# Optimization experiments

Hardware: AMD Instinct MI355X
Metric: run time of the kernel (lower is better)

## Reference

```python
import jax, jax.numpy as jnp
import numpy as np

N_NODES = 50000
N_EDGES = 1500000
FEAT = 128
CUTOFF = 5.0


def setup_inputs() -> dict:
    key = jax.random.key(0)
    k_x, k_ei, k_el, k_w = jax.random.split(key, 4)
    x = jax.random.normal(k_x, (N_NODES, FEAT), dtype=jnp.float32)
    edge_index = jax.random.randint(k_ei, (2, N_EDGES), 0, N_NODES, dtype=jnp.int64)
    edge_len = jax.random.uniform(k_el, (N_EDGES,), dtype=jnp.float32) * CUTOFF
    # learned params: equivariant mix (dense linear for scalar irreps, no bias),
    # log of distance scale (init sharpness=6.0), and 1->1 filter linear.
    W_mix = jax.random.normal(k_w, (FEAT, FEAT), dtype=jnp.float32) / np.sqrt(FEAT)
    log_scale = jnp.asarray(np.log(6.0), dtype=jnp.float32)
    filter_w = jnp.asarray(0.7, dtype=jnp.float32)
    filter_b = jnp.asarray(0.1, dtype=jnp.float32)
    return {"x": x, "edge_index": edge_index, "edge_len": edge_len,
            "W_mix": W_mix, "log_scale": log_scale,
            "filter_w": filter_w, "filter_b": filter_b}


def reference(x, edge_index, edge_len, W_mix, log_scale, filter_w, filter_b):
    sender = edge_index[0]
    receiver = edge_index[1]
    n_nodes = x.shape[0]

    scale = jnp.exp(log_scale).astype(edge_len.dtype)
    decay = jnp.exp(-jnp.maximum(edge_len / (scale + 1e-6), 0.0) ** 2)  # [E]
    gate = jax.nn.sigmoid(edge_len * filter_w + filter_b)               # [E]
    weights = jnp.nan_to_num(decay * gate, nan=0.0, posinf=0.0, neginf=0.0)

    # gather-scale-scatter: messages [E, F] -> per-node sum
    messages = weights[:, None].astype(x.dtype) * x[sender]
    agg = jax.ops.segment_sum(messages, receiver, num_segments=n_nodes)
    degree = jax.ops.segment_sum(jnp.ones_like(edge_len), receiver,
                                 num_segments=n_nodes)
    agg = agg / jnp.maximum(degree, 1.0)[:, None].astype(x.dtype)

    return x + agg @ W_mix
```

## Files before the change

kernel.cpp:

```cpp
#include <hip/hip_runtime.h>
#include <math.h>

#define FEAT 128
#define BSHIFT 5
#define BNODES 32
#define CAP 2048
#define EPB 8192
#define NBUCK_MAX 2048

__device__ __forceinline__ float edge_weight(float d, float scale, float fw, float fb) {
    float t = fmaxf(d / scale, 0.0f);
    float decay = expf(-t * t);
    float g = 1.0f / (1.0f + expf(-(d * fw + fb)));
    float w = decay * g;
    if (!isfinite(w)) w = 0.0f;
    return w;
}

__device__ __forceinline__ unsigned int bf16_rne(float f) {
    unsigned int b = __float_as_uint(f);
    return (b + 0x7FFFu + ((b >> 16) & 1u)) >> 16;
}

__global__ __launch_bounds__(256) void convert_kernel(const float4* __restrict__ x4,
                                                      uint2* __restrict__ xbf,
                                                      int n4) {
    int i = blockIdx.x * 256 + threadIdx.x;
    if (i >= n4) return;
    float4 v = x4[i];
    uint2 o;
    o.x = (bf16_rne(v.y) << 16) | bf16_rne(v.x);
    o.y = (bf16_rne(v.w) << 16) | bf16_rne(v.z);
    xbf[i] = o;
}

__global__ __launch_bounds__(256) void count_kernel(const int* __restrict__ recv,
                                                    int* __restrict__ boff,
                                                    int E, int nbuck) {
    __shared__ int cnt[NBUCK_MAX];
    int tid = threadIdx.x;
    for (int i = tid; i < nbuck; i += 256) cnt[i] = 0;
    __syncthreads();
    int base = blockIdx.x * EPB;
    int end = min(base + EPB, E);
    for (int e = base + tid; e < end; e += 256)
        atomicAdd(&cnt[recv[e] >> BSHIFT], 1);
    __syncthreads();
    for (int i = tid; i < nbuck; i += 256) {
        int c = cnt[i];
        if (c) atomicAdd(&boff[i + 1], c);
    }
}

__global__ __launch_bounds__(1024) void scan_kernel(int* __restrict__ off,
                                                    int* __restrict__ bcur, int M) {
    __shared__ int part[1024];
    int t = threadIdx.x;
    int chunk = (M + 1023) >> 10;
    int lo = t * chunk, hi = min(lo + chunk, M);
    int s = 0;
    for (int i = lo; i < hi; ++i) s += off[1 + i];
    part[t] = s;
    __syncthreads();
    for (int d = 1; d < 1024; d <<= 1) {
        int v = (t >= d) ? part[t - d] : 0;
        __syncthreads();
        part[t] += v;
        __syncthreads();
    }
    int run = part[t] - s;
    for (int i = lo; i < hi; ++i) {
        bcur[i] = run;
        run += off[1 + i];
        off[1 + i] = run;
    }
    if (t == 0) off[0] = 0;
}

__global__ __launch_bounds__(256) void bucket_scatter_kernel(
    const int* __restrict__ sender, const int* __restrict__ recv,
    const float* __restrict__ edge_len,
    const float* __restrict__ log_scale, const float* __restrict__ filter_w,
    const float* __restrict__ filter_b,
    int* __restrict__ bcur, unsigned long long* __restrict__ buf,
    int E, int nbuck) {
    __shared__ int cur[NBUCK_MAX];
    int tid = threadIdx.x;
    for (int i = tid; i < nbuck; i += 256) cur[i] = 0;
    __syncthreads();
    int base = blockIdx.x * EPB;
    int end = min(base + EPB, E);
    for (int e = base + tid; e < end; e += 256)
        atomicAdd(&cur[recv[e] >> BSHIFT], 1);
    __syncthreads();
    for (int i = tid; i < nbuck; i += 256) {
        int c = cur[i];
        cur[i] = c ? atomicAdd(&bcur[i], c) : 0;
    }
    __syncthreads();
    float scale = expf(log_scale[0]) + 1e-6f;
    float fw = filter_w[0], fb = filter_b[0];
    for (int e = base + tid; e < end; e += 256) {
        int r = recv[e];
        int s = sender[e];
        float w = edge_weight(edge_len[e], scale, fw, fb);
        int pos = atomicAdd(&cur[r >> BSHIFT], 1);
        unsigned long long rec = ((unsigned long long)__float_as_uint(w) << 32)
                               | (unsigned int)(s & 0xFFFF)
                               | ((unsigned int)(r & (BNODES - 1)) << 16);
        buf[pos] = rec;
    }
}

__device__ __forceinline__ void accum8(float acc[8], uint4 u, float w) {
    acc[0] = fmaf(w, __uint_as_float(u.x << 16), acc[0]);
    acc[1] = fmaf(w, __uint_as_float(u.x & 0xFFFF0000u), acc[1]);
    acc[2] = fmaf(w, __uint_as_float(u.y << 16), acc[2]);
    acc[3] = fmaf(w, __uint_as_float(u.y & 0xFFFF0000u), acc[3]);
    acc[4] = fmaf(w, __uint_as_float(u.z << 16), acc[4]);
    acc[5] = fmaf(w, __uint_as_float(u.z & 0xFFFF0000u), acc[5]);
    acc[6] = fmaf(w, __uint_as_float(u.w << 16), acc[6]);
    acc[7] = fmaf(w, __uint_as_float(u.w & 0xFFFF0000u), acc[7]);
}

__global__ __launch_bounds__(256) void bucket_sort_aggregate_kernel(
    const uint4* __restrict__ xbf4, const unsigned long long* __restrict__ buf,
    const int* __restrict__ boff, uint4* __restrict__ agg_bf4,
    int* __restrict__ deg, int N) {
    __shared__ unsigned long long recS[CAP];
    __shared__ int cnt32[BNODES];
    __shared__ int segoff[BNODES + 1];

    int b = blockIdx.x;
    int n0 = b << BSHIFT;
    int nEnd = min(n0 + BNODES, N);
    int lo = boff[b], hi = boff[b + 1];
    int tid = threadIdx.x;
    int lane = tid & 15;
    int grp = tid >> 4;

    float acc[2][8] = {{0.f,0.f,0.f,0.f,0.f,0.f,0.f,0.f},
                       {0.f,0.f,0.f,0.f,0.f,0.f,0.f,0.f}};
    int dcnt[2] = {0, 0};

    for (int pos = lo; pos < hi; pos += CAP) {
        int cnt = min(CAP, hi - pos);
        if (tid < BNODES) cnt32[tid] = 0;
        __syncthreads();

        unsigned long long rec[CAP / 256];
        int rnk[CAP / 256];
        int locl[CAP / 256];
#pragma unroll
        for (int k = 0; k < CAP / 256; ++k) {
            int i = k * 256 + tid;
            if (i < cnt) {
                unsigned long long r = buf[pos + i];
                int l = ((unsigned int)r >> 16) & (BNODES - 1);
                rec[k] = r;
                locl[k] = l;
                rnk[k] = atomicAdd(&cnt32[l], 1);
            }
        }
        __syncthreads();
        if (tid == 0) {
            int run = 0;
#pragma unroll
            for (int l = 0; l < BNODES; ++l) { segoff[l] = run; run += cnt32[l]; }
            segoff[BNODES] = run;
        }
        __syncthreads();
#pragma unroll
        for (int k = 0; k < CAP / 256; ++k) {
            int i = k * 256 + tid;
            if (i < cnt) recS[segoff[locl[k]] + rnk[k]] = rec[k];
        }
        __syncthreads();

#pragma unroll
        for (int which = 0; which < 2; ++which) {
            int l = grp + which * 16;
            int s0 = segoff[l], s1 = segoff[l + 1];
            dcnt[which] += s1 - s0;
            int i = s0;
            for (; i + 4 <= s1; i += 4) {
                unsigned long long r0 = recS[i];
                unsigned long long r1 = recS[i + 1];
                unsigned long long r2 = recS[i + 2];
                unsigned long long r3 = recS[i + 3];
                float w0 = __uint_as_float((unsigned int)(r0 >> 32));
                float w1 = __uint_as_float((unsigned int)(r1 >> 32));
                float w2 = __uint_as_float((unsigned int)(r2 >> 32));
                float w3 = __uint_as_float((unsigned int)(r3 >> 32));
                int s0i = (unsigned int)r0 & 0xFFFF;
                int s1i = (unsigned int)r1 & 0xFFFF;
                int s2i = (unsigned int)r2 & 0xFFFF;
                int s3i = (unsigned int)r3 & 0xFFFF;
                uint4 u0 = xbf4[(size_t)s0i * 16 + lane];
                uint4 u1 = xbf4[(size_t)s1i * 16 + lane];
                uint4 u2 = xbf4[(size_t)s2i * 16 + lane];
                uint4 u3 = xbf4[(size_t)s3i * 16 + lane];
                accum8(acc[which], u0, w0);
                accum8(acc[which], u1, w1);
                accum8(acc[which], u2, w2);
                accum8(acc[which], u3, w3);
            }
            for (; i < s1; ++i) {
                unsigned long long ra = recS[i];
                float wa = __uint_as_float((unsigned int)(ra >> 32));
                int sa = (unsigned int)ra & 0xFFFF;
                uint4 ua = xbf4[(size_t)sa * 16 + lane];
                accum8(acc[which], ua, wa);
            }
        }
        __syncthreads();
    }

#pragma unroll
    for (int which = 0; which < 2; ++which) {
        int n = n0 + grp + which * 16;
        if (n < nEnd) {
            uint4 o;
            o.x = (bf16_rne(acc[which][1]) << 16) | bf16_rne(acc[which][0]);
            o.y = (bf16_rne(acc[which][3]) << 16) | bf16_rne(acc[which][2]);
            o.z = (bf16_rne(acc[which][5]) << 16) | bf16_rne(acc[which][4]);
            o.w = (bf16_rne(acc[which][7]) << 16) | bf16_rne(acc[which][6]);
            agg_bf4[(size_t)n * 16 + lane] = o;
            if (lane == 0) deg[n] = dcnt[which];
        }
    }
}

__global__ __launch_bounds__(256) void finalize_kernel(
    const float* __restrict__ x, const uint4* __restrict__ agg_bf4,
    const int* __restrict__ deg, const float* __restrict__ Wm,
    float* __restrict__ out, int N) {
    __shared__ float aggS[64 * 128];
    __shared__ float Ws[128 * 64];
    const int n0 = blockIdx.x * 64;

    for (int i = threadIdx.x; i < 64 * 16; i += 256) {
        int r = i >> 4;
        int q = i & 15;
        int n = n0 + r;
        uint4 u = make_uint4(0u, 0u, 0u, 0u);
        if (n < N) u = agg_bf4[(size_t)n * 16 + q];
        float4 f0, f1;
        f0.x = __uint_as_float(u.x << 16);
        f0.y = __uint_as_float(u.x & 0xFFFF0000u);
        f0.z = __uint_as_float(u.y << 16);
        f0.w = __uint_as_float(u.y & 0xFFFF0000u);
        f1.x = __uint_as_float(u.z << 16);
        f1.y = __uint_as_float(u.z & 0xFFFF0000u);
        f1.z = __uint_as_float(u.w << 16);
        f1.w = __uint_as_float(u.w & 0xFFFF0000u);
        int m = (r >> 2) & 7;
        ((float4*)aggS)[r * 32 + ((2 * q) ^ m)] = f0;
        ((float4*)aggS)[r * 32 + ((2 * q + 1) ^ m)] = f1;
    }

    const int tc = threadIdx.x & 15;
    const int tr = threadIdx.x >> 4;

    float invd[4];
#pragma unroll
    for (int i = 0; i < 4; ++i) {
        int n = n0 + 4 * tr + i;
        float degf = 1.0f;
        if (n < N) degf = fmaxf((float)deg[n], 1.0f);
        invd[i] = 1.0f / degf;
    }

    for (int h = 0; h < 2; ++h) {
        for (int i = threadIdx.x; i < 128 * 16; i += 256) {
            int k = i >> 4;
            int j4 = i & 15;
            ((float4*)Ws)[k * 16 + j4] = ((const float4*)Wm)[k * 32 + h * 16 + j4];
        }
        __syncthreads();

        float acc[4][4];
#pragma unroll
        for (int i = 0; i < 4; ++i)
#pragma unroll
            for (int c = 0; c < 4; ++c) acc[i][c] = 0.f;

#pragma unroll 4
        for (int k0 = 0; k0 < 128; k0 += 4) {
            float4 ar4[4];
            const int chunk = (k0 >> 2) ^ (tr & 7);
#pragma unroll
            for (int i = 0; i < 4; ++i) {
                int r = 4 * tr + i;
                ar4[i] = ((const float4*)aggS)[r * 32 + chunk];
            }
            float4 wv4[4];
#pragma unroll
            for (int kk = 0; kk < 4; ++kk)
                wv4[kk] = *(const float4*)&Ws[(k0 + kk) * 64 + tc * 4];

            float wvv[4][4];
#pragma unroll
            for (int kk = 0; kk < 4; ++kk) {
                wvv[kk][0] = wv4[kk].x; wvv[kk][1] = wv4[kk].y;
                wvv[kk][2] = wv4[kk].z; wvv[kk][3] = wv4[kk].w;
            }
#pragma unroll
            for (int i = 0; i < 4; ++i) {
                float av[4] = {ar4[i].x, ar4[i].y, ar4[i].z, ar4[i].w};
#pragma unroll
                for (int kk = 0; kk < 4; ++kk)
#pragma unroll
                    for (int c = 0; c < 4; ++c)
                        acc[i][c] = fmaf(av[kk], wvv[kk][c], acc[i][c]);
            }
        }

#pragma unroll
        for (int i = 0; i < 4; ++i) {
            int n = n0 + 4 * tr + i;
            if (n < N) {
                size_t base = (size_t)n * FEAT + h * 64 + tc * 4;
                float4 xv = *(const float4*)&x[base];
                float4 o;
                o.x = xv.x + invd[i] * acc[i][0];
                o.y = xv.y + invd[i] * acc[i][1];
                o.z = xv.z + invd[i] * acc[i][2];
                o.w = xv.w + invd[i] * acc[i][3];
                *(float4*)&out[base] = o;
            }
        }
        __syncthreads();
    }
}

__global__ __launch_bounds__(256) void scatter_fallback(
    const float4* __restrict__ x4, const int* __restrict__ sender,
    const int* __restrict__ receiver, const float* __restrict__ edge_len,
    const float* __restrict__ log_scale, const float* __restrict__ filter_w,
    const float* __restrict__ filter_b, float* __restrict__ agg,
    float* __restrict__ deg, int E) {
    int gid = blockIdx.x * 256 + threadIdx.x;
    int e = gid >> 5;
    if (e >= E) return;
    int lane = gid & 31;
    int s = sender[e];
    int r = receiver[e];
    float scale = expf(log_scale[0]) + 1e-6f;
    float w = edge_weight(edge_len[e], scale, filter_w[0], filter_b[0]);
    float4 xv = x4[s * (FEAT / 4) + lane];
    float* dst = agg + (size_t)r * FEAT + lane * 4;
    unsafeAtomicAdd(dst + 0, w * xv.x);
    unsafeAtomicAdd(dst + 1, w * xv.y);
    unsafeAtomicAdd(dst + 2, w * xv.z);
    unsafeAtomicAdd(dst + 3, w * xv.w);
    if (lane == 0) unsafeAtomicAdd(&deg[r], 1.0f);
}

__global__ __launch_bounds__(256) void finalize_fallback(
    const float* __restrict__ x, const float* __restrict__ agg,
    const float* __restrict__ deg, const float* __restrict__ Wm,
    float* __restrict__ out, int N) {
    __shared__ float Wsf[FEAT * FEAT];
    for (int i = threadIdx.x * 4; i < FEAT * FEAT; i += 256 * 4)
        *(float4*)&Wsf[i] = *(const float4*)&Wm[i];
    __syncthreads();
    int half = threadIdx.x >> 7;
    int j = threadIdx.x & (FEAT - 1);
    for (int n0 = blockIdx.x * 2; n0 < N; n0 += gridDim.x * 2) {
        int n = n0 + half;
        if (n < N) {
            const float* arow = agg + (size_t)n * FEAT;
            float acc = 0.0f;
#pragma unroll 16
            for (int k = 0; k < FEAT; ++k) acc = fmaf(arow[k], Wsf[k * FEAT + j], acc);
            float invd = 1.0f / fmaxf(deg[n], 1.0f);
            size_t idx = (size_t)n * FEAT + j;
            out[idx] = x[idx] + invd * acc;
        }
    }
}

extern "C" void kernel_launch(void* const* d_in, const int* in_sizes, int n_in,
                              void* d_out, int out_size, void* d_ws, size_t ws_size,
                              hipStream_t stream) {
    const float* x         = (const float*)d_in[0];
    const int*   ei        = (const int*)d_in[1];
    const float* edge_len  = (const float*)d_in[2];
    const float* W_mix     = (const float*)d_in[3];
    const float* log_scale = (const float*)d_in[4];
    const float* filter_w  = (const float*)d_in[5];
    const float* filter_b  = (const float*)d_in[6];
    float* out = (float*)d_out;

    const int N = in_sizes[0] / FEAT;
    const int E = in_sizes[1] / 2;
    const int* sender   = ei;
    const int* receiver = ei + E;
    const int nbuck = (N + BNODES - 1) >> BSHIFT;

    size_t xbf_bytes  = (size_t)N * FEAT * 2;
    size_t aggb_bytes = (size_t)N * FEAT * 2;
    size_t buf_bytes  = (size_t)E * 8;
    size_t boff_bytes = (((size_t)(nbuck + 1) * 4) + 63) & ~(size_t)63;
    size_t bcur_bytes = (((size_t)nbuck * 4) + 63) & ~(size_t)63;
    size_t deg_bytes  = (((size_t)N * 4) + 63) & ~(size_t)63;
    size_t needed = xbf_bytes + aggb_bytes + buf_bytes + boff_bytes +
                    bcur_bytes + deg_bytes;

    if (ws_size >= needed && N <= 65536) {
        char* p = (char*)d_ws;
        uint2* xbf    = (uint2*)p;                        p += xbf_bytes;
        uint4* agg_bf = (uint4*)p;                        p += aggb_bytes;
        unsigned long long* buf = (unsigned long long*)p; p += buf_bytes;
        int* boff = (int*)p;                              p += boff_bytes;
        int* bcur = (int*)p;                              p += bcur_bytes;
        int* deg  = (int*)p;

        hipMemsetAsync(boff, 0, (size_t)(nbuck + 1) * 4, stream);

        int cblocks = (N * (FEAT / 4) + 255) / 256;
        convert_kernel<<<cblocks, 256, 0, stream>>>((const float4*)x, xbf,
                                                    N * (FEAT / 4));
        int chunkblocks = (E + EPB - 1) / EPB;
        count_kernel<<<chunkblocks, 256, 0, stream>>>(receiver, boff, E, nbuck);
        scan_kernel<<<1, 1024, 0, stream>>>(boff, bcur, nbuck);
        bucket_scatter_kernel<<<chunkblocks, 256, 0, stream>>>(
            sender, receiver, edge_len, log_scale, filter_w, filter_b,
            bcur, buf, E, nbuck);
        bucket_sort_aggregate_kernel<<<nbuck, 256, 0, stream>>>(
            (const uint4*)xbf, buf, boff, agg_bf, deg, N);
        int fblocks = (N + 63) / 64;
        finalize_kernel<<<fblocks, 256, 0, stream>>>(x, (const uint4*)agg_bf, deg,
                                                     W_mix, out, N);
    } else {
        float* agg = (float*)d_ws;
        float* degf = agg + (size_t)N * FEAT;
        hipMemsetAsync(agg, 0, ((size_t)N * FEAT + N) * sizeof(float), stream);
        int sblocks = (E * 32 + 255) / 256;
        scatter_fallback<<<sblocks, 256, 0, stream>>>(
            (const float4*)x, sender, receiver, edge_len,
            log_scale, filter_w, filter_b, agg, degf, E);
        finalize_fallback<<<512, 256, 0, stream>>>(x, agg, degf, W_mix, out, N);
    }
}
```

Before: 245.0 us.

## Replace global atomic bucket offsets with per-chunk count matrix and column scan

Count kernel now writes per-chunk bucket histograms to a matrix instead of atomically adding into global offsets. A new column-scan kernel turns these into per-chunk prefix offsets and bucket totals, which the single-block scan turns into bucket offsets. The scatter kernel loads its start positions directly, dropping its second histogram pass and the global atomics, and the memset goes away. It adds an extra kernel launch and a serial per-bucket loop over chunks, and it chooses the chunk size from the available workspace.

```diff
diff --git a/kernel.cpp b/kernel.cpp
--- a/kernel.cpp
+++ b/kernel.cpp
@@ -5,7 +5,6 @@
 #define BSHIFT 5
 #define BNODES 32
 #define CAP 2048
-#define EPB 8192
 #define NBUCK_MAX 2048
 
 __device__ __forceinline__ float edge_weight(float d, float scale, float fw, float fb) {
@@ -35,31 +34,44 @@
 }
 
 __global__ __launch_bounds__(256) void count_kernel(const int* __restrict__ recv,
-                                                    int* __restrict__ boff,
-                                                    int E, int nbuck) {
+                                                    int* __restrict__ sub,
+                                                    int E, int nbuck, int epb) {
     __shared__ int cnt[NBUCK_MAX];
     int tid = threadIdx.x;
     for (int i = tid; i < nbuck; i += 256) cnt[i] = 0;
     __syncthreads();
-    int base = blockIdx.x * EPB;
-    int end = min(base + EPB, E);
+    int base = blockIdx.x * epb;
+    int end = min(base + epb, E);
     for (int e = base + tid; e < end; e += 256)
         atomicAdd(&cnt[recv[e] >> BSHIFT], 1);
     __syncthreads();
-    for (int i = tid; i < nbuck; i += 256) {
-        int c = cnt[i];
-        if (c) atomicAdd(&boff[i + 1], c);
-    }
-}
-
-__global__ __launch_bounds__(1024) void scan_kernel(int* __restrict__ off,
-                                                    int* __restrict__ bcur, int M) {
+    size_t row = (size_t)blockIdx.x * nbuck;
+    for (int i = tid; i < nbuck; i += 256) sub[row + i] = cnt[i];
+}
+
+__global__ __launch_bounds__(256) void colscan_kernel(int* __restrict__ sub,
+                                                      int* __restrict__ tot,
+                                                      int nbuck, int nchunk) {
+    int b = blockIdx.x * 256 + threadIdx.x;
+    if (b >= nbuck) return;
+    int run = 0;
+    for (int c = 0; c < nchunk; ++c) {
+        size_t idx = (size_t)c * nbuck + b;
+        int v = sub[idx];
+        sub[idx] = run;
+        run += v;
+    }
+    tot[b] = run;
+}
+
+__global__ __launch_bounds__(1024) void scan_kernel(const int* __restrict__ tot,
+                                                    int* __restrict__ boff, int M) {
     __shared__ int part[1024];
     int t = threadIdx.x;
     int chunk = (M + 1023) >> 10;
     int lo = t * chunk, hi = min(lo + chunk, M);
     int s = 0;
-    for (int i = lo; i < hi; ++i) s += off[1 + i];
+    for (int i = lo; i < hi; ++i) s += tot[i];
     part[t] = s;
     __syncthreads();
     for (int d = 1; d < 1024; d <<= 1) {
@@ -70,11 +82,10 @@
     }
     int run = part[t] - s;
     for (int i = lo; i < hi; ++i) {
-        bcur[i] = run;
-        run += off[1 + i];
-        off[1 + i] = run;
-    }
-    if (t == 0) off[0] = 0;
+        boff[i] = run;
+        run += tot[i];
+    }
+    if (hi == M) boff[M] = run;
 }
 
 __global__ __launch_bounds__(256) void bucket_scatter_kernel(
@@ -82,22 +93,15 @@
     const float* __restrict__ edge_len,
     const float* __restrict__ log_scale, const float* __restrict__ filter_w,
     const float* __restrict__ filter_b,
-    int* __restrict__ bcur, unsigned long long* __restrict__ buf,
-    int E, int nbuck) {
+    const int* __restrict__ sub, const int* __restrict__ boff,
+    unsigned long long* __restrict__ buf, int E, int nbuck, int epb) {
     __shared__ int cur[NBUCK_MAX];
     int tid = threadIdx.x;
-    for (int i = tid; i < nbuck; i += 256) cur[i] = 0;
+    size_t row = (size_t)blockIdx.x * nbuck;
+    for (int i = tid; i < nbuck; i += 256) cur[i] = boff[i] + sub[row + i];
     __syncthreads();
-    int base = blockIdx.x * EPB;
-    int end = min(base + EPB, E);
-    for (int e = base + tid; e < end; e += 256)
-        atomicAdd(&cur[recv[e] >> BSHIFT], 1);
-    __syncthreads();
-    for (int i = tid; i < nbuck; i += 256) {
-        int c = cur[i];
-        cur[i] = c ? atomicAdd(&bcur[i], c) : 0;
-    }
-    __syncthreads();
+    int base = blockIdx.x * epb;
+    int end = min(base + epb, E);
     float scale = expf(log_scale[0]) + 1e-6f;
     float fw = filter_w[0], fb = filter_b[0];
     for (int e = base + tid; e < end; e += 256) {
@@ -402,32 +406,42 @@
     size_t xbf_bytes  = (size_t)N * FEAT * 2;
     size_t aggb_bytes = (size_t)N * FEAT * 2;
     size_t buf_bytes  = (size_t)E * 8;
+    size_t tot_bytes  = (((size_t)nbuck * 4) + 63) & ~(size_t)63;
     size_t boff_bytes = (((size_t)(nbuck + 1) * 4) + 63) & ~(size_t)63;
-    size_t bcur_bytes = (((size_t)nbuck * 4) + 63) & ~(size_t)63;
     size_t deg_bytes  = (((size_t)N * 4) + 63) & ~(size_t)63;
-    size_t needed = xbf_bytes + aggb_bytes + buf_bytes + boff_bytes +
-                    bcur_bytes + deg_bytes;
-
-    if (ws_size >= needed && N <= 65536) {
+    size_t fixed = xbf_bytes + aggb_bytes + buf_bytes + tot_bytes + boff_bytes +
+                   deg_bytes;
+
+    int epb = 0, nchunk = 0;
+    size_t sub_bytes = 0;
+    const int epb_opts[3] = {4096, 8192, 16384};
+    for (int oi = 0; oi < 3; ++oi) {
+        int cand = epb_opts[oi];
+        int nc = (E + cand - 1) / cand;
+        size_t sb = (((size_t)nc * nbuck * 4) + 63) & ~(size_t)63;
+        if (fixed + sb <= ws_size) { epb = cand; nchunk = nc; sub_bytes = sb; break; }
+    }
+
+    if (epb != 0 && N <= 65536) {
         char* p = (char*)d_ws;
         uint2* xbf    = (uint2*)p;                        p += xbf_bytes;
         uint4* agg_bf = (uint4*)p;                        p += aggb_bytes;
         unsigned long long* buf = (unsigned long long*)p; p += buf_bytes;
+        int* sub  = (int*)p;                              p += sub_bytes;
+        int* tot  = (int*)p;                              p += tot_bytes;
         int* boff = (int*)p;                              p += boff_bytes;
-        int* bcur = (int*)p;                              p += bcur_bytes;
         int* deg  = (int*)p;
-
-        hipMemsetAsync(boff, 0, (size_t)(nbuck + 1) * 4, stream);
 
         int cblocks = (N * (FEAT / 4) + 255) / 256;
         convert_kernel<<<cblocks, 256, 0, stream>>>((const float4*)x, xbf,
                                                     N * (FEAT / 4));
-        int chunkblocks = (E + EPB - 1) / EPB;
-        count_kernel<<<chunkblocks, 256, 0, stream>>>(receiver, boff, E, nbuck);
-        scan_kernel<<<1, 1024, 0, stream>>>(boff, bcur, nbuck);
-        bucket_scatter_kernel<<<chunkblocks, 256, 0, stream>>>(
+        count_kernel<<<nchunk, 256, 0, stream>>>(receiver, sub, E, nbuck, epb);
+        colscan_kernel<<<(nbuck + 255) / 256, 256, 0, stream>>>(sub, tot,
+                                                                nbuck, nchunk);
+        scan_kernel<<<1, 1024, 0, stream>>>(tot, boff, nbuck);
+        bucket_scatter_kernel<<<nchunk, 256, 0, stream>>>(
             sender, receiver, edge_len, log_scale, filter_w, filter_b,
-            bcur, buf, E, nbuck);
+            sub, boff, buf, E, nbuck, epb);
         bucket_sort_aggregate_kernel<<<nbuck, 256, 0, stream>>>(
             (const uint4*)xbf, buf, boff, agg_bf, deg, N);
         int fblocks = (N + 63) / 64;
```

After: 308.4 us. +25.9%, slower.
